# Kernel optimization log

Hardware: AMD Instinct MI355X
Metric: run time of the kernel (lower is better)

The kernel has to match this reference:

```python
import jax, jax.numpy as jnp
import numpy as np

EPS = 1e-5
NEG_SLOPE = 0.1


def _edgeconv_layer(x, ev, W, gamma, beta):
    # x: [B, C, G], ev: [B, 3, G], W: [O, 2C+3]
    cat = jnp.concatenate([x, x - x[:, :, :1], ev], axis=1)  # [B, 2C+3, G]
    y = jnp.einsum('oc,bcg->bog', W, cat)                     # 1x1 conv, no bias
    # BatchNorm2d (training mode: batch stats over B and spatial=G dims)
    m = jnp.mean(y, axis=(0, 2), keepdims=True)
    v = jnp.mean((y - m) ** 2, axis=(0, 2), keepdims=True)
    y = gamma[None, :, None] * ((y - m) * jax.lax.rsqrt(v + EPS)) + beta[None, :, None]
    return jnp.where(y >= 0, y, NEG_SLOPE * y)                # LeakyReLU(0.1)


def setup_inputs() -> dict:
    key = jax.random.key(0)
    ks = jax.random.split(key, 7)
    B, Cin, Cout, G = 32, 64, 128, 8192
    inp = {
        'features': jax.random.normal(ks[0], (B, Cin, G), dtype=jnp.float32),
        'edge_vectors': jax.random.normal(ks[1], (B, 3, G), dtype=jnp.float32),
        'W1': jax.random.normal(ks[2], (Cout, Cin * 2 + 3), dtype=jnp.float32) * 0.05,
        'W2': jax.random.normal(ks[3], (Cout, Cout * 2 + 3), dtype=jnp.float32) * 0.05,
        'W3': jax.random.normal(ks[4], (Cout, Cout * 2 + 3), dtype=jnp.float32) * 0.05,
        'W4': jax.random.normal(ks[5], (Cout, Cout * 2 + 3), dtype=jnp.float32) * 0.05,
    }
    for i in range(1, 5):
        inp[f'g{i}'] = jnp.ones((Cout,), dtype=jnp.float32)
        inp[f'b{i}'] = jnp.zeros((Cout,), dtype=jnp.float32)
    return inp


def reference(features, edge_vectors, W1, W2, W3, W4, g1, g2, g3, g4, b1, b2, b3, b4):
    x = features
    for W, g, b in ((W1, g1, b1), (W2, g2, b2), (W3, g3, b3), (W4, g4, b4)):
        x = _edgeconv_layer(x, edge_vectors, W, g, b)
    return jnp.max(x, axis=-1)  # [B, Cout]
```

## Files before the change

kernel.cpp:

```cpp
#include <hip/hip_runtime.h>
#include <string.h>

#define G 8192
#define B 32
#define O 128
#define NBLK 2048
#define NTOT 262144.0f

typedef float f32x4 __attribute__((ext_vector_type(4)));
typedef _Float16 half8 __attribute__((ext_vector_type(8)));
typedef _Float16 half4 __attribute__((ext_vector_type(4)));
typedef _Float16 half2v __attribute__((ext_vector_type(2)));

__device__ __forceinline__ float lrelu(float v) { return fmaxf(v, 0.1f * v); }

__device__ __forceinline__ unsigned pack2h(float lo, float hi) {
    half2v t; t.x = (_Float16)lo; t.y = (_Float16)hi;
    return __builtin_bit_cast(unsigned, t);
}

__device__ __forceinline__ void wfrag_one(const float* __restrict__ W, int ldw, int K, int KS,
                                          _Float16* __restrict__ out, int idx) {
    int j = idx & 7, lane = (idx >> 3) & 63, t = idx >> 9;
    int kk = t % KS, m8 = t / KS;
    int o = m8 * 16 + (lane & 15);
    int k = kk * 32 + ((lane >> 4) & 3) * 4 + (j & 3) + (j >> 2) * 16;
    float v;
    if (k < K)          v = W[o * ldw + k] + W[o * ldw + K + k];
    else if (k < K + 3) v = W[o * ldw + 2 * K + (k - K)];
    else                v = 0.f;
    out[idx] = (_Float16)v;
}

__global__ void prep_all(const float* __restrict__ W1, const float* __restrict__ W2,
                         const float* __restrict__ W3, const float* __restrict__ W4,
                         _Float16* __restrict__ wf1, _Float16* __restrict__ wf2,
                         _Float16* __restrict__ wf3, _Float16* __restrict__ wf4) {
    int idx = blockIdx.x * 256 + threadIdx.x;
    if (idx < 12288)                wfrag_one(W1, 131, 64, 3, wf1, idx);
    else if (idx < 12288 + 20480)   wfrag_one(W2, 259, 128, 5, wf2, idx - 12288);
    else if (idx < 12288 + 40960)   wfrag_one(W3, 259, 128, 5, wf3, idx - 12288 - 20480);
    else if (idx < 12288 + 61440)   wfrag_one(W4, 259, 128, 5, wf4, idx - 12288 - 40960);
}

__global__ void bias0_first(const float* __restrict__ X, const float* __restrict__ W,
                            float* __restrict__ bias) {
    __shared__ float x0[64];
    int b = blockIdx.x, o = threadIdx.x;
    if (o < 64) x0[o] = X[((size_t)b * 64 + o) * G];
    __syncthreads();
    float acc = 0.f;
    for (int c = 0; c < 64; ++c) acc += W[o * 131 + 64 + c] * x0[c];
    bias[b * O + o] = -acc;
}

__global__ void bias0_next(const _Float16* __restrict__ Y, const float* __restrict__ A,
                           const float* __restrict__ Cc, const float* __restrict__ W,
                           float* __restrict__ bias) {
    __shared__ float xn[128];
    int b = blockIdx.x, o = threadIdx.x;
    float v = (float)Y[((size_t)b * O + o) * G];
    xn[o] = lrelu(A[o] * v + Cc[o]);
    __syncthreads();
    float acc = 0.f;
    for (int c = 0; c < 128; ++c) acc += W[o * 259 + 128 + c] * xn[c];
    bias[b * O + o] = -acc;
}

template<int K, int KS, bool NORM, bool F32IN>
__global__ __launch_bounds__(256) void edge_mfma(
    const void* __restrict__ Xin_,
    _Float16* __restrict__ Yout,
    const _Float16* __restrict__ Wf,
    const float* __restrict__ bias,
    const float* __restrict__ An, const float* __restrict__ Cn,
    const float* __restrict__ EV,
    float* __restrict__ part)
{
    constexpr int KP  = KS * 32;
    constexpr int NHW = KS * 512 + 24;
    static_assert(KP >= K + 3, "pad");
    __shared__ __align__(16) _Float16 lds[8 * NHW];

    const int tid  = threadIdx.x;
    const int lane = tid & 63;
    const int wave = tid >> 6;
    const int gt   = blockIdx.x;
    const int b    = blockIdx.y;
    const int g0   = gt * 128;
    const int bid  = b * 64 + gt;

    const float* Xf = (const float*)Xin_;
    const _Float16* Xh = (const _Float16*)Xin_;

    {
        const int c0 = lane * 2;
        const int KGS = KP / 4;
        for (int kg = wave; kg < KGS; kg += 4) {
            float va[4], vb[4];
            const int kbase = kg * 4;
            if (kbase < K) {
#pragma unroll
                for (int r = 0; r < 4; ++r) {
                    int k = kbase + r;
                    float x0, x1;
                    if (F32IN) {
                        const float* src = Xf + ((size_t)b * K + k) * G + g0 + c0;
                        x0 = src[0]; x1 = src[1];
                    } else {
                        const _Float16* src = Xh + ((size_t)b * K + k) * G + g0 + c0;
                        x0 = (float)src[0]; x1 = (float)src[1];
                    }
                    if (NORM) {
                        float a = An[k], cc = Cn[k];
                        x0 = lrelu(a * x0 + cc);
                        x1 = lrelu(a * x1 + cc);
                    }
                    va[r] = x0; vb[r] = x1;
                }
            } else {
#pragma unroll
                for (int r = 0; r < 4; ++r) {
                    int e = kbase + r - K;
                    if (e >= 0 && e < 3) {
                        const float* src = EV + ((size_t)b * 3 + e) * G + g0 + c0;
                        va[r] = src[0]; vb[r] = src[1];
                    } else { va[r] = 0.f; vb[r] = 0.f; }
                }
            }
            half4 ha, hb;
#pragma unroll
            for (int r = 0; r < 4; ++r) { ha[r] = (_Float16)va[r]; hb[r] = (_Float16)vb[r]; }
            const int kk = kg >> 3, jh = (kg >> 2) & 1, l16 = kg & 3;
            {
                int c = c0, q = c >> 3, n16 = c & 7;
                int off = n16 * NHW + kk * 512 + (q + l16 * 16) * 8 + jh * 4;
                *(half4*)(&lds[off]) = ha;
            }
            {
                int c = c0 + 1, q = c >> 3, n16 = c & 7;
                int off = n16 * NHW + kk * 512 + (q + l16 * 16) * 8 + jh * 4;
                *(half4*)(&lds[off]) = hb;
            }
        }
    }
    __syncthreads();

    half8 af[2][KS];
#pragma unroll
    for (int m = 0; m < 2; ++m)
#pragma unroll
        for (int kk = 0; kk < KS; ++kk)
            af[m][kk] = *(const half8*)(Wf + (((wave * 2 + m) * KS + kk) * 64 + lane) * 8);

    f32x4 acc[2][8];
#pragma unroll
    for (int m = 0; m < 2; ++m)
#pragma unroll
        for (int n = 0; n < 8; ++n) acc[m][n] = (f32x4){0.f, 0.f, 0.f, 0.f};

#pragma unroll
    for (int kk = 0; kk < KS; ++kk) {
#pragma unroll
        for (int n = 0; n < 8; ++n) {
            half8 bf = *(const half8*)(&lds[n * NHW + kk * 512 + lane * 8]);
            acc[0][n] = __builtin_amdgcn_mfma_f32_16x16x32_f16(af[0][kk], bf, acc[0][n], 0, 0, 0);
            acc[1][n] = __builtin_amdgcn_mfma_f32_16x16x32_f16(af[1][kk], bf, acc[1][n], 0, 0, 0);
        }
    }

    const int ob = wave * 32;
    const int fq = lane >> 4, fr = lane & 15;
#pragma unroll
    for (int m = 0; m < 2; ++m) {
        float4 bv = *(const float4*)(bias + b * O + ob + m * 16 + fq * 4);
#pragma unroll
        for (int n = 0; n < 8; ++n) {
            acc[m][n].x += bv.x; acc[m][n].y += bv.y;
            acc[m][n].z += bv.z; acc[m][n].w += bv.w;
        }
    }
#pragma unroll
    for (int m = 0; m < 2; ++m) {
#pragma unroll
        for (int i = 0; i < 4; ++i) {
            float s = 0.f, q = 0.f;
#pragma unroll
            for (int n = 0; n < 8; ++n) {
                float v = acc[m][n][i];
                s += v; q += v * v;
            }
            s += __shfl_xor(s, 1, 64); q += __shfl_xor(q, 1, 64);
            s += __shfl_xor(s, 2, 64); q += __shfl_xor(q, 2, 64);
            s += __shfl_xor(s, 4, 64); q += __shfl_xor(q, 4, 64);
            s += __shfl_xor(s, 8, 64); q += __shfl_xor(q, 8, 64);
            if (fr == 0) {
                int o = ob + m * 16 + fq * 4 + i;
                part[bid * 256 + o]       = s;
                part[bid * 256 + 128 + o] = q;
            }
            uint4 w;
            w.x = pack2h(acc[m][0][i], acc[m][1][i]);
            w.y = pack2h(acc[m][2][i], acc[m][3][i]);
            w.z = pack2h(acc[m][4][i], acc[m][5][i]);
            w.w = pack2h(acc[m][6][i], acc[m][7][i]);
            size_t row = (size_t)b * O + ob + m * 16 + fq * 4 + i;
            *reinterpret_cast<uint4*>(Yout + row * G + g0 + fr * 8) = w;
        }
    }
}

__global__ void finalize(const float* __restrict__ part, const float* __restrict__ gamma,
                         const float* __restrict__ beta, float* __restrict__ A,
                         float* __restrict__ Cc) {
    __shared__ float rs[256], rq[256];
    int o = blockIdx.x, t = threadIdx.x;
    float s = 0.f, q = 0.f;
    for (int bid = t; bid < NBLK; bid += 256) {
        s += part[bid * 256 + o];
        q += part[bid * 256 + 128 + o];
    }
    rs[t] = s; rq[t] = q;
    __syncthreads();
    for (int w = 128; w > 0; w >>= 1) {
        if (t < w) { rs[t] += rs[t + w]; rq[t] += rq[t + w]; }
        __syncthreads();
    }
    if (t == 0) {
        float mean = rs[0] / NTOT;
        float var  = rq[0] / NTOT - mean * mean;
        float a = gamma[o] * rsqrtf(var + 1e-5f);
        A[o]  = a;
        Cc[o] = beta[o] - mean * a;
    }
}

__global__ void maxout(const _Float16* __restrict__ Y, const float* __restrict__ A,
                       const float* __restrict__ Cc, float* __restrict__ out) {
    int w    = blockIdx.x * 4 + (threadIdx.x >> 6);
    int lane = threadIdx.x & 63;
    int b = w >> 7, o = w & 127;
    float a = A[o], cc = Cc[o];
    const _Float16* row = Y + ((size_t)b * O + o) * G;
    float m = -3.4e38f;
    for (int j = lane * 8; j < G; j += 512) {
        uint4 v = *reinterpret_cast<const uint4*>(row + j);
#pragma unroll
        for (int p = 0; p < 4; ++p) {
            unsigned u = (&v.x)[p];
            half2v h = __builtin_bit_cast(half2v, u);
            m = fmaxf(m, lrelu(a * (float)h.x + cc));
            m = fmaxf(m, lrelu(a * (float)h.y + cc));
        }
    }
    for (int d = 32; d > 0; d >>= 1) m = fmaxf(m, __shfl_down(m, d, 64));
    if (lane == 0) out[b * O + o] = m;
}

extern "C" void kernel_launch(void* const* d_in, const int* in_sizes, int n_in,
                              void* d_out, int out_size, void* d_ws, size_t ws_size,
                              hipStream_t stream) {
    const float* feat = (const float*)d_in[0];
    const float* ev   = (const float*)d_in[1];
    const float* W1   = (const float*)d_in[2];
    const float* W2   = (const float*)d_in[3];
    const float* W3   = (const float*)d_in[4];
    const float* W4   = (const float*)d_in[5];
    const float* g1   = (const float*)d_in[6];
    const float* b1   = (const float*)d_in[7];
    const float* g2   = (const float*)d_in[8];
    const float* b2   = (const float*)d_in[9];
    const float* g3   = (const float*)d_in[10];
    const float* b3   = (const float*)d_in[11];
    const float* g4   = (const float*)d_in[12];
    const float* b4   = (const float*)d_in[13];

    _Float16* y   = (_Float16*)d_ws;
    _Float16* wf1 = y + 33554432;
    _Float16* wf2 = wf1 + 12288;
    _Float16* wf3 = wf2 + 20480;
    _Float16* wf4 = wf3 + 20480;
    float* bias = (float*)(wf4 + 20480);
    float* Aar  = bias + 4096;
    float* Car  = Aar + 128;
    float* part = Car + 128;

    dim3 mg(64, 32);
    prep_all<<<288, 256, 0, stream>>>(W1, W2, W3, W4, wf1, wf2, wf3, wf4);
    bias0_first<<<32, 128, 0, stream>>>(feat, W1, bias);

    edge_mfma<64, 3, false, true><<<mg, 256, 0, stream>>>(feat, y, wf1, bias, Aar, Car, ev, part);
    finalize<<<128, 256, 0, stream>>>(part, g1, b1, Aar, Car);

    bias0_next<<<32, 128, 0, stream>>>(y, Aar, Car, W2, bias);
    edge_mfma<128, 5, true, false><<<mg, 256, 0, stream>>>(y, y, wf2, bias, Aar, Car, ev, part);
    finalize<<<128, 256, 0, stream>>>(part, g2, b2, Aar, Car);

    bias0_next<<<32, 128, 0, stream>>>(y, Aar, Car, W3, bias);
    edge_mfma<128, 5, true, false><<<mg, 256, 0, stream>>>(y, y, wf3, bias, Aar, Car, ev, part);
    finalize<<<128, 256, 0, stream>>>(part, g3, b3, Aar, Car);

    bias0_next<<<32, 128, 0, stream>>>(y, Aar, Car, W4, bias);
    edge_mfma<128, 5, true, false><<<mg, 256, 0, stream>>>(y, y, wf4, bias, Aar, Car, ev, part);
    finalize<<<128, 256, 0, stream>>>(part, g4, b4, Aar, Car);

    maxout<<<1024, 256, 0, stream>>>(y, Aar, Car, (float*)d_out);
}
```

Before: 327.8 us.

## Switch activations to point-major fp16 layout with fused edge-vector channels

Activations move from channel-major [B,O,G] to point-major [B,G,136] fp16, with the edge vectors stored in spare channels 128..130. A transpose kernel converts the first-layer input. Each edge_mfma block can then copy its tile straight into LDS with 16-byte loads, instead of gathering strided channels and converting them. Normalization and LeakyReLU now run in packed fp16 on the B fragments, and maxout uses a max/min trick keyed on the sign of the scale. The risks are the extra transpose pass, reduced precision from applying BN in fp16, and partial-stat rows doubling to 4096.

```diff
diff --git a/kernel.cpp b/kernel.cpp
--- a/kernel.cpp
+++ b/kernel.cpp
@@ -1,15 +1,13 @@
 #include <hip/hip_runtime.h>
-#include <string.h>
 
 #define G 8192
 #define B 32
 #define O 128
-#define NBLK 2048
+#define NROWS 4096
 #define NTOT 262144.0f
 
 typedef float f32x4 __attribute__((ext_vector_type(4)));
 typedef _Float16 half8 __attribute__((ext_vector_type(8)));
-typedef _Float16 half4 __attribute__((ext_vector_type(4)));
 typedef _Float16 half2v __attribute__((ext_vector_type(2)));
 
 __device__ __forceinline__ float lrelu(float v) { return fmaxf(v, 0.1f * v); }
@@ -22,9 +20,9 @@
 __device__ __forceinline__ void wfrag_one(const float* __restrict__ W, int ldw, int K, int KS,
                                           _Float16* __restrict__ out, int idx) {
     int j = idx & 7, lane = (idx >> 3) & 63, t = idx >> 9;
-    int kk = t % KS, m8 = t / KS;
-    int o = m8 * 16 + (lane & 15);
-    int k = kk * 32 + ((lane >> 4) & 3) * 4 + (j & 3) + (j >> 2) * 16;
+    int kk = t % KS, m16 = t / KS;
+    int o = m16 * 16 + (lane & 15);
+    int k = kk * 32 + ((lane >> 4) & 3) * 8 + j;
     float v;
     if (k < K)          v = W[o * ldw + k] + W[o * ldw + K + k];
     else if (k < K + 3) v = W[o * ldw + 2 * K + (k - K)];
@@ -43,6 +41,35 @@
     else if (idx < 12288 + 61440)   wfrag_one(W4, 259, 128, 5, wf4, idx - 12288 - 40960);
 }
 
+__global__ __launch_bounds__(256) void transpose_in(
+    const float* __restrict__ F, const float* __restrict__ EV,
+    _Float16* __restrict__ xT, _Float16* __restrict__ Y) {
+    __shared__ _Float16 tl[128 * 72];
+    const int t = threadIdx.x, gblk = blockIdx.x, b = blockIdx.y;
+    const int g0 = gblk * 128;
+    for (int idx = t; idx < 8192; idx += 256) {
+        int c = idx >> 7, gi = idx & 127;
+        tl[gi * 72 + c] = (_Float16)F[((size_t)b * 64 + c) * G + g0 + gi];
+    }
+    __syncthreads();
+    const int gi = t >> 1, h = t & 1;
+    _Float16* dst = xT + ((size_t)b * G + g0 + gi) * 80;
+#pragma unroll
+    for (int j = 0; j < 4; ++j)
+        *(half8*)(dst + h * 32 + j * 8) = *(const half8*)(tl + gi * 72 + h * 32 + j * 8);
+    if (h == 0) {
+        float e0 = EV[((size_t)b * 3 + 0) * G + g0 + gi];
+        float e1 = EV[((size_t)b * 3 + 1) * G + g0 + gi];
+        float e2 = EV[((size_t)b * 3 + 2) * G + g0 + gi];
+        half8 ev8 = {};
+        ev8[0] = (_Float16)e0; ev8[1] = (_Float16)e1; ev8[2] = (_Float16)e2;
+        half8 z = {};
+        *(half8*)(dst + 64) = ev8;
+        *(half8*)(dst + 72) = z;
+        *(half8*)(Y + ((size_t)b * G + g0 + gi) * 136 + 128) = ev8;
+    }
+}
+
 __global__ void bias0_first(const float* __restrict__ X, const float* __restrict__ W,
                             float* __restrict__ bias) {
     __shared__ float x0[64];
@@ -59,7 +86,7 @@
                            float* __restrict__ bias) {
     __shared__ float xn[128];
     int b = blockIdx.x, o = threadIdx.x;
-    float v = (float)Y[((size_t)b * O + o) * G];
+    float v = (float)Y[((size_t)b * G) * 136 + o];
     xn[o] = lrelu(A[o] * v + Cc[o]);
     __syncthreads();
     float acc = 0.f;
@@ -67,158 +94,123 @@
     bias[b * O + o] = -acc;
 }
 
-template<int K, int KS, bool NORM, bool F32IN>
+template<int KS, int SXI, int SXO, bool NORM>
 __global__ __launch_bounds__(256) void edge_mfma(
-    const void* __restrict__ Xin_,
-    _Float16* __restrict__ Yout,
+    const _Float16* __restrict__ X,
+    _Float16* __restrict__ Y,
     const _Float16* __restrict__ Wf,
     const float* __restrict__ bias,
-    const float* __restrict__ An, const float* __restrict__ Cn,
-    const float* __restrict__ EV,
+    const _Float16* __restrict__ Ah, const _Float16* __restrict__ Ch,
     float* __restrict__ part)
 {
-    constexpr int KP  = KS * 32;
-    constexpr int NHW = KS * 512 + 24;
-    static_assert(KP >= K + 3, "pad");
-    __shared__ __align__(16) _Float16 lds[8 * NHW];
-
+    __shared__ _Float16 lds[128 * SXI + 32];
     const int tid  = threadIdx.x;
     const int lane = tid & 63;
     const int wave = tid >> 6;
-    const int gt   = blockIdx.x;
+    const int fr   = lane & 15;
+    const int grp  = lane >> 4;
+    const int p      = wave & 1;
+    const int mhalf  = wave >> 1;
+    const int gblk = blockIdx.x;
     const int b    = blockIdx.y;
-    const int g0   = gt * 128;
-    const int bid  = b * 64 + gt;
-
-    const float* Xf = (const float*)Xin_;
-    const _Float16* Xh = (const _Float16*)Xin_;
-
-    {
-        const int c0 = lane * 2;
-        const int KGS = KP / 4;
-        for (int kg = wave; kg < KGS; kg += 4) {
-            float va[4], vb[4];
-            const int kbase = kg * 4;
-            if (kbase < K) {
-#pragma unroll
-                for (int r = 0; r < 4; ++r) {
-                    int k = kbase + r;
-                    float x0, x1;
-                    if (F32IN) {
-                        const float* src = Xf + ((size_t)b * K + k) * G + g0 + c0;
-                        x0 = src[0]; x1 = src[1];
-                    } else {
-                        const _Float16* src = Xh + ((size_t)b * K + k) * G + g0 + c0;
-                        x0 = (float)src[0]; x1 = (float)src[1];
-                    }
-                    if (NORM) {
-                        float a = An[k], cc = Cn[k];
-                        x0 = lrelu(a * x0 + cc);
-                        x1 = lrelu(a * x1 + cc);
-                    }
-                    va[r] = x0; vb[r] = x1;
-                }
-            } else {
-#pragma unroll
-                for (int r = 0; r < 4; ++r) {
-                    int e = kbase + r - K;
-                    if (e >= 0 && e < 3) {
-                        const float* src = EV + ((size_t)b * 3 + e) * G + g0 + c0;
-                        va[r] = src[0]; vb[r] = src[1];
-                    } else { va[r] = 0.f; vb[r] = 0.f; }
-                }
+    const int g0   = gblk * 128;
+
+    constexpr int BYTES = 128 * SXI * 2;
+    constexpr int NIT = (BYTES + 4095) / 4096;
+    const char* src = (const char*)(X + ((size_t)b * G + g0) * SXI);
+#pragma unroll
+    for (int it = 0; it < NIT; ++it) {
+        int off = it * 4096 + tid * 16;
+        if (BYTES % 4096 == 0 || off < BYTES)
+            *(uint4*)((char*)lds + off) = *(const uint4*)(src + off);
+    }
+    __syncthreads();
+
+    half8 af[4][KS];
+#pragma unroll
+    for (int mf = 0; mf < 4; ++mf)
+#pragma unroll
+        for (int kk = 0; kk < KS; ++kk)
+            af[mf][kk] = *(const half8*)(Wf + ((((mhalf * 4 + mf) * KS) + kk) * 64 + lane) * 8);
+
+    half8 ah[KS > 1 ? KS - 1 : 1], ch[KS > 1 ? KS - 1 : 1];
+    if (NORM) {
+#pragma unroll
+        for (int kk = 0; kk < KS - 1; ++kk) {
+            ah[kk] = *(const half8*)(Ah + kk * 32 + grp * 8);
+            ch[kk] = *(const half8*)(Ch + kk * 32 + grp * 8);
+        }
+    }
+
+    f32x4 sacc[4], qacc[4];
+#pragma unroll
+    for (int mf = 0; mf < 4; ++mf) { sacc[mf] = (f32x4)0.f; qacc[mf] = (f32x4)0.f; }
+
+#pragma unroll
+    for (int nfl = 0; nfl < 4; ++nfl) {
+        const int nf = p * 4 + nfl;
+        const int grow = nf * 16 + fr;
+        f32x4 acc[4];
+#pragma unroll
+        for (int mf = 0; mf < 4; ++mf) acc[mf] = (f32x4)0.f;
+
+#pragma unroll
+        for (int kk = 0; kk < KS; ++kk) {
+            half8 bf = *(const half8*)(lds + grow * SXI + kk * 32 + grp * 8);
+            if (NORM && kk < KS - 1) {
+                half8 t = bf * ah[kk] + ch[kk];
+                bf = __builtin_elementwise_max(t, t * (_Float16)0.1f);
             }
-            half4 ha, hb;
-#pragma unroll
-            for (int r = 0; r < 4; ++r) { ha[r] = (_Float16)va[r]; hb[r] = (_Float16)vb[r]; }
-            const int kk = kg >> 3, jh = (kg >> 2) & 1, l16 = kg & 3;
-            {
-                int c = c0, q = c >> 3, n16 = c & 7;
-                int off = n16 * NHW + kk * 512 + (q + l16 * 16) * 8 + jh * 4;
-                *(half4*)(&lds[off]) = ha;
+            if (kk == KS - 1) {
+                if (grp != 0) bf = (half8)((_Float16)0);
             }
-            {
-                int c = c0 + 1, q = c >> 3, n16 = c & 7;
-                int off = n16 * NHW + kk * 512 + (q + l16 * 16) * 8 + jh * 4;
-                *(half4*)(&lds[off]) = hb;
-            }
-        }
-    }
-    __syncthreads();
-
-    half8 af[2][KS];
-#pragma unroll
-    for (int m = 0; m < 2; ++m)
-#pragma unroll
-        for (int kk = 0; kk < KS; ++kk)
-            af[m][kk] = *(const half8*)(Wf + (((wave * 2 + m) * KS + kk) * 64 + lane) * 8);
-
-    f32x4 acc[2][8];
-#pragma unroll
-    for (int m = 0; m < 2; ++m)
-#pragma unroll
-        for (int n = 0; n < 8; ++n) acc[m][n] = (f32x4){0.f, 0.f, 0.f, 0.f};
-
-#pragma unroll
-    for (int kk = 0; kk < KS; ++kk) {
-#pragma unroll
-        for (int n = 0; n < 8; ++n) {
-            half8 bf = *(const half8*)(&lds[n * NHW + kk * 512 + lane * 8]);
-            acc[0][n] = __builtin_amdgcn_mfma_f32_16x16x32_f16(af[0][kk], bf, acc[0][n], 0, 0, 0);
-            acc[1][n] = __builtin_amdgcn_mfma_f32_16x16x32_f16(af[1][kk], bf, acc[1][n], 0, 0, 0);
-        }
-    }
-
-    const int ob = wave * 32;
-    const int fq = lane >> 4, fr = lane & 15;
-#pragma unroll
-    for (int m = 0; m < 2; ++m) {
-        float4 bv = *(const float4*)(bias + b * O + ob + m * 16 + fq * 4);
-#pragma unroll
-        for (int n = 0; n < 8; ++n) {
-            acc[m][n].x += bv.x; acc[m][n].y += bv.y;
-            acc[m][n].z += bv.z; acc[m][n].w += bv.w;
-        }
-    }
-#pragma unroll
-    for (int m = 0; m < 2; ++m) {
+#pragma unroll
+            for (int mf = 0; mf < 4; ++mf)
+                acc[mf] = __builtin_amdgcn_mfma_f32_16x16x32_f16(af[mf][kk], bf, acc[mf], 0, 0, 0);
+        }
+
+#pragma unroll
+        for (int mf = 0; mf < 4; ++mf) {
+            float4 bv = *(const float4*)(bias + b * O + mhalf * 64 + mf * 16 + grp * 4);
+            acc[mf][0] += bv.x; acc[mf][1] += bv.y; acc[mf][2] += bv.z; acc[mf][3] += bv.w;
+            sacc[mf] += acc[mf];
+            qacc[mf] += acc[mf] * acc[mf];
+            uint2 w;
+            w.x = pack2h(acc[mf][0], acc[mf][1]);
+            w.y = pack2h(acc[mf][2], acc[mf][3]);
+            *(uint2*)(Y + ((size_t)b * G + g0 + grow) * SXO + mhalf * 64 + mf * 16 + grp * 4) = w;
+        }
+    }
+
+    const int row = ((b * 64 + gblk) * 2 + p) * 256;
+#pragma unroll
+    for (int mf = 0; mf < 4; ++mf) {
 #pragma unroll
         for (int i = 0; i < 4; ++i) {
-            float s = 0.f, q = 0.f;
-#pragma unroll
-            for (int n = 0; n < 8; ++n) {
-                float v = acc[m][n][i];
-                s += v; q += v * v;
-            }
+            float s = sacc[mf][i], q = qacc[mf][i];
             s += __shfl_xor(s, 1, 64); q += __shfl_xor(q, 1, 64);
             s += __shfl_xor(s, 2, 64); q += __shfl_xor(q, 2, 64);
             s += __shfl_xor(s, 4, 64); q += __shfl_xor(q, 4, 64);
             s += __shfl_xor(s, 8, 64); q += __shfl_xor(q, 8, 64);
             if (fr == 0) {
-                int o = ob + m * 16 + fq * 4 + i;
-                part[bid * 256 + o]       = s;
-                part[bid * 256 + 128 + o] = q;
+                int o = mhalf * 64 + mf * 16 + grp * 4 + i;
+                part[row + o]       = s;
+                part[row + 128 + o] = q;
             }
-            uint4 w;
-            w.x = pack2h(acc[m][0][i], acc[m][1][i]);
-            w.y = pack2h(acc[m][2][i], acc[m][3][i]);
-            w.z = pack2h(acc[m][4][i], acc[m][5][i]);
-            w.w = pack2h(acc[m][6][i], acc[m][7][i]);
-            size_t row = (size_t)b * O + ob + m * 16 + fq * 4 + i;
-            *reinterpret_cast<uint4*>(Yout + row * G + g0 + fr * 8) = w;
         }
     }
 }
 
 __global__ void finalize(const float* __restrict__ part, const float* __restrict__ gamma,
                          const float* __restrict__ beta, float* __restrict__ A,
-                         float* __restrict__ Cc) {
+                         float* __restrict__ Cc, _Float16* __restrict__ Ahh,
+                         _Float16* __restrict__ Chh) {
     __shared__ float rs[256], rq[256];
     int o = blockIdx.x, t = threadIdx.x;
     float s = 0.f, q = 0.f;
-    for (int bid = t; bid < NBLK; bid += 256) {
-        s += part[bid * 256 + o];
-        q += part[bid * 256 + 128 + o];
+    for (int r = t; r < NROWS; r += 256) {
+        s += part[r * 256 + o];
+        q += part[r * 256 + 128 + o];
     }
     rs[t] = s; rq[t] = q;
     __syncthreads();
@@ -230,31 +222,40 @@
         float mean = rs[0] / NTOT;
         float var  = rq[0] / NTOT - mean * mean;
         float a = gamma[o] * rsqrtf(var + 1e-5f);
-        A[o]  = a;
-        Cc[o] = beta[o] - mean * a;
-    }
-}
-
-__global__ void maxout(const _Float16* __restrict__ Y, const float* __restrict__ A,
-                       const float* __restrict__ Cc, float* __restrict__ out) {
-    int w    = blockIdx.x * 4 + (threadIdx.x >> 6);
-    int lane = threadIdx.x & 63;
-    int b = w >> 7, o = w & 127;
-    float a = A[o], cc = Cc[o];
-    const _Float16* row = Y + ((size_t)b * O + o) * G;
-    float m = -3.4e38f;
-    for (int j = lane * 8; j < G; j += 512) {
-        uint4 v = *reinterpret_cast<const uint4*>(row + j);
-#pragma unroll
-        for (int p = 0; p < 4; ++p) {
-            unsigned u = (&v.x)[p];
-            half2v h = __builtin_bit_cast(half2v, u);
-            m = fmaxf(m, lrelu(a * (float)h.x + cc));
-            m = fmaxf(m, lrelu(a * (float)h.y + cc));
-        }
-    }
-    for (int d = 32; d > 0; d >>= 1) m = fmaxf(m, __shfl_down(m, d, 64));
-    if (lane == 0) out[b * O + o] = m;
+        float c = beta[o] - mean * a;
+        A[o] = a; Cc[o] = c;
+        Ahh[o] = (_Float16)a; Chh[o] = (_Float16)c;
+    }
+}
+
+__global__ __launch_bounds__(1024) void maxout(const _Float16* __restrict__ Y,
+                                               const float* __restrict__ A,
+                                               const float* __restrict__ Cc,
+                                               float* __restrict__ out) {
+    __shared__ _Float16 smx[64 * 136], smn[64 * 136];
+    const int t = threadIdx.x, b = blockIdx.x;
+    const int o8 = (t & 15) * 8, gs = t >> 4;
+    const _Float16* base = Y + ((size_t)b * G) * 136 + o8;
+    half8 mx = *(const half8*)(base + (size_t)gs * 136);
+    half8 mn = mx;
+    for (int g = gs + 64; g < G; g += 64) {
+        half8 v = *(const half8*)(base + (size_t)g * 136);
+        mx = __builtin_elementwise_max(mx, v);
+        mn = __builtin_elementwise_min(mn, v);
+    }
+    *(half8*)(smx + gs * 136 + o8) = mx;
+    *(half8*)(smn + gs * 136 + o8) = mn;
+    __syncthreads();
+    if (t < 128) {
+        float vmx = -3.4e38f, vmn = 3.4e38f;
+        for (int i = 0; i < 64; ++i) {
+            vmx = fmaxf(vmx, (float)smx[i * 136 + t]);
+            vmn = fminf(vmn, (float)smn[i * 136 + t]);
+        }
+        float a = A[t], c = Cc[t];
+        float v = (a >= 0.f ? vmx : vmn);
+        out[b * O + t] = lrelu(a * v + c);
+    }
 }
 
 extern "C" void kernel_launch(void* const* d_in, const int* in_sizes, int n_in,
@@ -275,34 +276,38 @@
     const float* g4   = (const float*)d_in[12];
     const float* b4   = (const float*)d_in[13];
 
-    _Float16* y   = (_Float16*)d_ws;
-    _Float16* wf1 = y + 33554432;
+    _Float16* y  = (_Float16*)d_ws;
+    _Float16* xT = y + 35651648;
+    float* part  = (float*)(xT + 20971584);
+    float* bias  = part + 1048576;
+    float* Aar   = bias + 4096;
+    float* Car   = Aar + 128;
+    _Float16* wf1 = (_Float16*)(Car + 128);
     _Float16* wf2 = wf1 + 12288;
     _Float16* wf3 = wf2 + 20480;
     _Float16* wf4 = wf3 + 20480;
-    float* bias = (float*)(wf4 + 20480);
-    float* Aar  = bias + 4096;
-    float* Car  = Aar + 128;
-    float* part = Car + 128;
-
-    dim3 mg(64, 32);
+    _Float16* Ah  = wf4 + 20480;
+    _Float16* Ch  = Ah + 192;
+
+    dim3 tg(64, 32);
     prep_all<<<288, 256, 0, stream>>>(W1, W2, W3, W4, wf1, wf2, wf3, wf4);
+    transpose_in<<<tg, 256, 0, stream>>>(feat, ev, xT, y);
     bias0_first<<<32, 128, 0, stream>>>(feat, W1, bias);
 
-    edge_mfma<64, 3, false, true><<<mg, 256, 0, stream>>>(feat, y, wf1, bias, Aar, Car, ev, part);
-    finalize<<<128, 256, 0, stream>>>(part, g1, b1, Aar, Car);
+    edge_mfma<3, 80, 136, false><<<tg, 256, 0, stream>>>(xT, y, wf1, bias, Ah, Ch, part);
+    finalize<<<128, 256, 0, stream>>>(part, g1, b1, Aar, Car, Ah, Ch);
 
     bias0_next<<<32, 128, 0, stream>>>(y, Aar, Car, W2, bias);
-    edge_mfma<128, 5, true, false><<<mg, 256, 0, stream>>>(y, y, wf2, bias, Aar, Car, ev, part);
-    finalize<<<128, 256, 0, stream>>>(part, g2, b2, Aar, Car);
+    edge_mfma<5, 136, 136, true><<<tg, 256, 0, stream>>>(y, y, wf2, bias, Ah, Ch, part);
+    finalize<<<128, 256, 0, stream>>>(part, g2, b2, Aar, Car, Ah, Ch);
 
     bias0_next<<<32, 128, 0, stream>>>(y, Aar, Car, W3, bias);
-    edge_mfma<128, 5, true, false><<<mg, 256, 0, stream>>>(y, y, wf3, bias, Aar, Car, ev, part);
-    finalize<<<128, 256, 0, stream>>>(part, g3, b3, Aar, Car);
+    edge_mfma<5, 136, 136, true><<<tg, 256, 0, stream>>>(y, y, wf3, bias, Ah, Ch, part);
+    finalize<<<128, 256, 0, stream>>>(part, g3, b3, Aar, Car, Ah, Ch);
 
     bias0_next<<<32, 128, 0, stream>>>(y, Aar, Car, W4, bias);
-    edge_mfma<128, 5, true, false><<<mg, 256, 0, stream>>>(y, y, wf4, bias, Aar, Car, ev, part);
-    finalize<<<128, 256, 0, stream>>>(part, g4, b4, Aar, Car);
-
-    maxout<<<1024, 256, 0, stream>>>(y, Aar, Car, (float*)d_out);
-}
+    edge_mfma<5, 136, 136, true><<<tg, 256, 0, stream>>>(y, y, wf4, bias, Ah, Ch, part);
+    finalize<<<128, 256, 0, stream>>>(part, g4, b4, Aar, Car, Ah, Ch);
+
+    maxout<<<32, 1024, 0, stream>>>(y, Aar, Car, (float*)d_out);
+}
```

After: 429.8 us. 31.1% more time.
